# Optimization experiments

Measured on AMD Instinct MI355X. Metric: run time of the kernel, lower is better.

Reference implementation:

```python
import jax, jax.numpy as jnp
import numpy as np

PHI = 0.1  # fraction of pruned weights randomized per inference


def setup_inputs() -> dict:
    key = jax.random.key(0)
    k1, k2, k3 = jax.random.split(key, 3)
    d_out, d_in, batch = 8192, 8192, 256
    W = jax.random.normal(k1, (d_out, d_in), jnp.float32) * 0.02
    prune = jax.random.uniform(k2, (d_out, d_in)) < 0.9
    W = jnp.where(prune, 0.0, W)
    mask = (W == 0.0)  # _register_masks: pruned positions
    x = jax.random.normal(k3, (batch, d_in), jnp.float32)
    return {"x": x, "W": W, "mask": mask}


def reference(x, W, mask):
    # --- _apply_random_flip (vectorized) ---
    n_pruned = int(np.asarray(jnp.sum(mask)))          # concrete mask -> static count
    n_flip = max(1, int(PHI * n_pruned))
    keep = ~mask
    n_keep = jnp.sum(keep).astype(W.dtype)
    wk = jnp.where(keep, W, 0.0)
    mean = jnp.sum(wk) / n_keep
    # torch .std() is unbiased (n-1 denominator)
    var = jnp.sum(jnp.where(keep, (W - mean) ** 2, 0.0)) / (n_keep - 1.0)
    std = jnp.sqrt(var)
    key = jax.random.key(42)
    ks, kv = jax.random.split(key)
    # uniform random permutation of pruned indices -> top_k of random scores
    scores = jnp.where(mask.ravel(), jax.random.uniform(ks, (W.size,)), -1.0)
    _, flip_idx = jax.lax.top_k(scores, n_flip)        # [n_flip] flat indices into W
    vals = jax.random.normal(kv, (n_flip,), W.dtype) * std * 0.1
    W_flipped = W.ravel().at[flip_idx].set(vals).reshape(W.shape)
    # --- base_model forward (Linear, no bias) ---
    out = x @ W_flipped.T                               # [batch, d_out]
    # --- _restore_masks: zero flipped weights again (no effect on out) ---
    _ = jnp.where(mask, 0.0, W_flipped)
    return out
```

## Files before the change

### kernel.cpp

```cpp
#include <hip/hip_runtime.h>

typedef unsigned int u32;
typedef unsigned long long u64;
typedef unsigned short u16;

#define NTOT   67108864u
#define T0P    7399424u
#define PBASE  7226u
#define NSUP   966u
#define SEGN   2048u
#define SEGCAP 4096u
#define SUPCAP 8192u
#define KSPLIT 4

struct Scalars {
  double sumW;
  double sumW2;
  u64 npruned;
  u64 nflip;
  float stdf;
  float pad;
};

#define OFF_GHIST  0ull
#define OFF_ALLOC  4096ull
#define OFF_SBASE  8192ull
#define OFF_SCUR   12288ull
#define OFF_SC     16384ull
#define OFF_SEGCNT 16512ull
#define OFF_XBF    24704ull
#define OFF_SEGS   4219008ull
#define OFF_ROUTED 37773440ull

__host__ __device__ inline void tf2x32(u32 k0, u32 k1, u32 x0, u32 x1, u32& y0, u32& y1) {
  u32 ks2 = k0 ^ k1 ^ 0x1BD11BDAu;
  x0 += k0; x1 += k1;
#define TFR(r) { x0 += x1; x1 = (x1 << (r)) | (x1 >> (32 - (r))); x1 ^= x0; }
  TFR(13) TFR(15) TFR(26) TFR(6)  x0 += k1;  x1 += ks2 + 1u;
  TFR(17) TFR(29) TFR(16) TFR(24) x0 += ks2; x1 += k0 + 2u;
  TFR(13) TFR(15) TFR(26) TFR(6)  x0 += k0;  x1 += k1 + 3u;
  TFR(17) TFR(29) TFR(16) TFR(24) x0 += k1;  x1 += ks2 + 4u;
  TFR(13) TFR(15) TFR(26) TFR(6)  x0 += ks2; x1 += k0 + 5u;
#undef TFR
  y0 = x0; y1 = x1;
}

__device__ inline u32 jax_bits32(u32 k0, u32 k1, u32 i) {
  u32 y0, y1; tf2x32(k0, k1, 0u, i, y0, y1);
  return y0 ^ y1;
}

__device__ inline u16 f2bf(float f) {
  union { float f; u32 u; } c; c.f = f;
  u32 r = ((c.u >> 16) & 1u) + 0x7FFFu;
  return (u16)((c.u + r) >> 16);
}

__device__ inline float erfinv32(float x) {
  float w = -log1pf(-x * x);
  float p;
  if (w < 5.0f) {
    w -= 2.5f;
    p = 2.81022636e-08f;
    p = fmaf(p, w, 3.43273939e-07f);
    p = fmaf(p, w, -3.5233877e-06f);
    p = fmaf(p, w, -4.39150654e-06f);
    p = fmaf(p, w, 0.00021858087f);
    p = fmaf(p, w, -0.00125372503f);
    p = fmaf(p, w, -0.00417768164f);
    p = fmaf(p, w, 0.246640727f);
    p = fmaf(p, w, 1.50140941f);
  } else {
    w = sqrtf(w) - 3.0f;
    p = -0.000200214257f;
    p = fmaf(p, w, 0.000100950558f);
    p = fmaf(p, w, 0.00134934322f);
    p = fmaf(p, w, -0.00367342844f);
    p = fmaf(p, w, 0.00573950773f);
    p = fmaf(p, w, -0.0076224613f);
    p = fmaf(p, w, 0.00943887047f);
    p = fmaf(p, w, 1.00167406f);
    p = fmaf(p, w, 2.83297682f);
  }
  return p * x;
}

__device__ inline void blk_excl_scan_1024(const u32* cnt, u32* excl, u32* wtmp) {
  __syncthreads();
  u32 t = threadIdx.x;
  u32 a0 = cnt[t*4], a1 = cnt[t*4+1], a2 = cnt[t*4+2], a3 = cnt[t*4+3];
  u32 s = a0 + a1 + a2 + a3;
  u32 lane = t & 63, wv = t >> 6;
  u32 inc = s;
  for (int o = 1; o < 64; o <<= 1) { u32 v = (u32)__shfl_up((int)inc, o); if (lane >= (u32)o) inc += v; }
  if (lane == 63) wtmp[wv] = inc;
  __syncthreads();
  u32 woff = 0;
  for (u32 w = 0; w < wv; w++) woff += wtmp[w];
  u32 base = woff + inc - s;
  excl[t*4]   = base;
  excl[t*4+1] = base + a0;
  excl[t*4+2] = base + a0 + a1;
  excl[t*4+3] = base + a0 + a1 + a2;
  __syncthreads();
}

__device__ inline void blk_suffix_scan_1024(const u32* cnt, u32* suf, u32* wtmp) {
  __syncthreads();
  u32 t = threadIdx.x;
  u32 a0 = cnt[1023 - t*4], a1 = cnt[1022 - t*4], a2 = cnt[1021 - t*4], a3 = cnt[1020 - t*4];
  u32 s = a0 + a1 + a2 + a3;
  u32 lane = t & 63, wv = t >> 6;
  u32 inc = s;
  for (int o = 1; o < 64; o <<= 1) { u32 v = (u32)__shfl_up((int)inc, o); if (lane >= (u32)o) inc += v; }
  if (lane == 63) wtmp[wv] = inc;
  __syncthreads();
  u32 woff = 0;
  for (u32 w = 0; w < wv; w++) woff += wtmp[w];
  u32 base = woff + inc - s;
  suf[1023 - t*4] = base;
  suf[1022 - t*4] = base + a0;
  suf[1021 - t*4] = base + a1 + a0;
  suf[1020 - t*4] = base + a2 + a1 + a0;
  __syncthreads();
}

__global__ __launch_bounds__(256) void k_pass1(const float* __restrict__ W, Scalars* sc,
                                               u32* ghist, u32* segcnt, u32* segs,
                                               u32 uk0, u32 uk1) {
  __shared__ u32 lhist[1024];
  __shared__ u32 lcnt, lwr;
  for (u32 j = threadIdx.x; j < 1024; j += 256) lhist[j] = 0;
  if (threadIdx.x == 0) { lcnt = 0; lwr = 0; }
  __syncthreads();
  u32 gid = blockIdx.x * 256 + threadIdx.x;
  u32 stride4 = SEGN * 256 * 4;
  u32 lane = threadIdx.x & 63;
  u64 lt = (lane == 0) ? 0ull : (~0ull >> (64 - lane));
  u32* seg = segs + (u64)blockIdx.x * SEGCAP;
  double s = 0.0, s2 = 0.0; u32 cnt = 0;
  for (u32 b4 = gid * 4; b4 < NTOT; b4 += stride4) {
    float4 wv4 = *(const float4*)(W + b4);
    float we[4] = {wv4.x, wv4.y, wv4.z, wv4.w};
#pragma unroll
    for (int e = 0; e < 4; e++) {
      u32 l = b4 + e;
      float w = we[e];
      s  += (double)w;
      s2 += (double)w * w;
      bool pr = (w == 0.0f);
      cnt += pr ? 1u : 0u;
      u32 sb = jax_bits32(uk0, uk1, l) >> 9;
      bool q = pr && (sb >= T0P);
      u64 m = __ballot(q);
      u32 tot = (u32)__popcll(m);
      if (tot) {
        u32 base = 0;
        if (lane == 0) base = atomicAdd(&lcnt, tot);
        base = (u32)__shfl((int)base, 0);
        if (base + tot <= SEGCAP) {
          if (lane == 0) atomicMax(&lwr, base + tot);
          if (q) {
            seg[base + (u32)__popcll(m & lt)] = l;
            atomicAdd(&lhist[(sb >> 10) - PBASE], 1u);
          }
        }
      }
    }
  }
  for (int o = 32; o > 0; o >>= 1) {
    s += __shfl_down(s, o); s2 += __shfl_down(s2, o); cnt += __shfl_down(cnt, o);
  }
  if (lane == 0) {
    atomicAdd(&sc->sumW, s);
    atomicAdd(&sc->sumW2, s2);
    atomicAdd(&sc->npruned, (u64)cnt);
  }
  __syncthreads();
  for (u32 j = threadIdx.x; j < 1024; j += 256)
    if (j < NSUP && lhist[j]) atomicAdd(&ghist[j], lhist[j]);
  if (threadIdx.x == 0) segcnt[blockIdx.x] = lwr;
}

__global__ __launch_bounds__(256) void k_scan(const u32* __restrict__ ghist, Scalars* sc,
                                              u32* alloc, u32* superbase, u32* supercur) {
  __shared__ u32 h[1024], ex[1024], sb[1024], wtmp[4];
  u32 t = threadIdx.x;
  for (u32 j = t; j < 1024; j += 256) h[j] = ghist[j];
  blk_excl_scan_1024(h, ex, wtmp);
  blk_suffix_scan_1024(h, sb, wtmp);
  for (u32 j = t; j < 1024; j += 256) {
    alloc[j] = ex[j]; superbase[j] = sb[j]; supercur[j] = ex[j];
  }
  if (t == 0) {
    double nk = (double)NTOT - (double)sc->npruned;
    double mean = sc->sumW / nk;
    double var = (sc->sumW2 - 2.0 * mean * sc->sumW + nk * mean * mean) / (nk - 1.0);
    sc->stdf = (float)sqrt(var);
    u64 nfi = (u64)(0.1 * (double)sc->npruned);
    if (nfi < 1) nfi = 1;
    sc->nflip = nfi;
  }
}

__global__ __launch_bounds__(256) void k_route(const u32* __restrict__ segs,
                                               const u32* __restrict__ segcnt,
                                               u32* supercur, u32* routed,
                                               u32 uk0, u32 uk1) {
  __shared__ u32 lbuf[16384];
  __shared__ u16 lp[16384];
  __shared__ u16 inv[16384];
  __shared__ u32 lhist[1024], lbase[1024], gdest[1024], lcur[1024];
  __shared__ u32 wtmp[4];
  u32 t = threadIdx.x;
  for (u32 j = t; j < 1024; j += 256) lhist[j] = 0;
  u32 c0 = segcnt[blockIdx.x*4+0], c1 = segcnt[blockIdx.x*4+1];
  u32 c2 = segcnt[blockIdx.x*4+2], c3 = segcnt[blockIdx.x*4+3];
  u32 off[4] = {0, c0, c0+c1, c0+c1+c2};
  u32 cs[4] = {c0, c1, c2, c3};
  u32 total = c0+c1+c2+c3;
  __syncthreads();
#pragma unroll
  for (int sg = 0; sg < 4; sg++) {
    const u32* sp = segs + ((u64)blockIdx.x*4 + sg) * SEGCAP;
    for (u32 i = t; i < cs[sg]; i += 256) {
      u32 idx = sp[i];
      u32 sb2 = jax_bits32(uk0, uk1, idx) >> 9;
      u32 p = (sb2 >> 10) - PBASE;
      u32 j = off[sg] + i;
      lbuf[j] = idx;
      lp[j] = (u16)p;
      atomicAdd(&lhist[p], 1u);
    }
  }
  blk_excl_scan_1024(lhist, lbase, wtmp);
  for (u32 p = t; p < 1024; p += 256) {
    u32 c = lhist[p];
    if (c) gdest[p] = atomicAdd(&supercur[p], c);
    lcur[p] = lbase[p];
  }
  __syncthreads();
  for (u32 j = t; j < total; j += 256) {
    u32 slot = atomicAdd(&lcur[lp[j]], 1u);
    inv[slot] = (u16)j;
  }
  __syncthreads();
  for (u32 j = t; j < total; j += 256) {
    u32 i = inv[j];
    u32 p = lp[i];
    routed[gdest[p] + (j - lbase[p])] = lbuf[i];
  }
}

__global__ __launch_bounds__(256) void k_rank(float* __restrict__ W,
                                              const u32* __restrict__ ghist,
                                              const u32* __restrict__ alloc,
                                              const u32* __restrict__ superbase,
                                              const u32* __restrict__ routed,
                                              const Scalars* __restrict__ sc,
                                              u32 uk0, u32 uk1, u32 vk0, u32 vk1) {
  u32 p = blockIdx.x;
  u32 n = ghist[p]; if (n == 0) return;
  if (n > SUPCAP) n = SUPCAP;
  u64 nflip = sc->nflip;
  u32 rbase = superbase[p];
  if ((u64)rbase >= nflip) return;
  __shared__ u32 sIdx[SUPCAP];
  __shared__ u16 sFine[SUPCAP];
  __shared__ u32 pIdx[SUPCAP];
  __shared__ u32 hist[1024], gbase[1024], cur[1024];
  __shared__ u32 wtmp[4];
  u32 t = threadIdx.x;
  for (u32 j = t; j < 1024; j += 256) hist[j] = 0;
  __syncthreads();
  const u32* src = routed + alloc[p];
  u32 fbias = (p + PBASE) << 10;
  for (u32 i = t; i < n; i += 256) {
    u32 idx = src[i];
    u32 sb2 = jax_bits32(uk0, uk1, idx) >> 9;
    u32 f = sb2 - fbias;
    sIdx[i] = idx;
    sFine[i] = (u16)f;
    atomicAdd(&hist[f], 1u);
  }
  blk_suffix_scan_1024(hist, gbase, wtmp);
  for (u32 j = t; j < 1024; j += 256) cur[j] = gbase[j];
  __syncthreads();
  for (u32 i = t; i < n; i += 256) {
    u32 pos = atomicAdd(&cur[sFine[i]], 1u);
    pIdx[pos] = sIdx[i];
  }
  __syncthreads();
  float stdf = sc->stdf;
  for (u32 i = t; i < n; i += 256) {
    u32 f = sFine[i];
    u32 g0 = gbase[f], g1 = g0 + hist[f];
    u32 v = sIdx[i];
    u32 ord = 0;
    for (u32 q = g0; q < g1; q++) ord += (pIdx[q] < v) ? 1u : 0u;
    u64 rank = (u64)rbase + gbase[f] + ord;
    if (rank >= nflip) continue;
    u32 bits = jax_bits32(vk0, vk1, (u32)rank);
    union { u32 u; float fl; } cv; cv.u = 0x3F800000u | (bits >> 9);
    float fu = cv.fl - 1.0f;
    const float lo = -0.99999994f;
    float u2 = fmaxf(lo, fu * 2.0f + lo);
    float nrm = 1.41421354f * erfinv32(u2);
    W[v] = (nrm * stdf) * 0.1f;
  }
}

__global__ __launch_bounds__(256) void k_xconv(const float* __restrict__ x, u16* __restrict__ xbf) {
  u32 i = blockIdx.x * blockDim.x + threadIdx.x;
  float4 v = ((const float4*)x)[i];
  ushort4 o; o.x = f2bf(v.x); o.y = f2bf(v.y); o.z = f2bf(v.z); o.w = f2bf(v.w);
  ((ushort4*)xbf)[i] = o;
}

typedef __bf16 bf16x8 __attribute__((ext_vector_type(8)));
typedef float f32x4 __attribute__((ext_vector_type(4)));

__global__ __launch_bounds__(256, 2) void k_gemm(const u16* __restrict__ xbf,
                                                 const float* __restrict__ W,
                                                 float* __restrict__ out) {
  __shared__ u16 xs[256 * 72];
  __shared__ u16 wsm[64 * 72];
  u32 tid = threadIdx.x;
  u32 lane = tid & 63, wv = tid >> 6;
  u32 nt0 = blockIdx.x * 64;
  u32 kbase = blockIdx.y * (8192 / KSPLIT);
  f32x4 acc[4][4];
#pragma unroll
  for (int i = 0; i < 4; i++)
#pragma unroll
    for (int j = 0; j < 4; j++) acc[i][j] = (f32x4){0.f, 0.f, 0.f, 0.f};

  for (u32 kb = kbase; kb < kbase + 2048u; kb += 64u) {
#pragma unroll
    for (int r8 = 0; r8 < 8; r8++) {
      u32 row = r8 * 32 + (tid >> 3);
      u32 kseg = (tid & 7) * 8;
      uint4 v = *(const uint4*)(xbf + (u64)row * 8192 + kb + kseg);
      *(uint4*)&xs[row * 72 + kseg] = v;
    }
#pragma unroll
    for (int r = 0; r < 4; r++) {
      u32 f4 = r * 256 + tid;
      u32 row = f4 >> 4;
      u32 kc = (f4 & 15) * 4;
      float4 v = *(const float4*)(W + (u64)(nt0 + row) * 8192 + kb + kc);
      ushort4 o; o.x = f2bf(v.x); o.y = f2bf(v.y); o.z = f2bf(v.z); o.w = f2bf(v.w);
      *(ushort4*)&wsm[row * 72 + kc] = o;
    }
    __syncthreads();
#pragma unroll
    for (int ks = 0; ks < 2; ks++) {
      bf16x8 a[4], b[4];
      u32 koff = ks * 32 + (lane >> 4) * 8;
      u32 rsel = lane & 15;
#pragma unroll
      for (int mt = 0; mt < 4; mt++) a[mt] = *(bf16x8*)&xs[(wv * 64 + mt * 16 + rsel) * 72 + koff];
#pragma unroll
      for (int nt = 0; nt < 4; nt++) b[nt] = *(bf16x8*)&wsm[(nt * 16 + rsel) * 72 + koff];
#pragma unroll
      for (int mt = 0; mt < 4; mt++)
#pragma unroll
        for (int nt = 0; nt < 4; nt++)
          acc[mt][nt] = __builtin_amdgcn_mfma_f32_16x16x32_bf16(a[mt], b[nt], acc[mt][nt], 0, 0, 0);
    }
    __syncthreads();
  }
  u32 quad = lane >> 4, col = lane & 15;
#pragma unroll
  for (int mt = 0; mt < 4; mt++)
#pragma unroll
    for (int nt = 0; nt < 4; nt++) {
      u32 n = nt0 + nt * 16 + col;
#pragma unroll
      for (int rg = 0; rg < 4; rg++) {
        u32 m = wv * 64 + mt * 16 + quad * 4 + rg;
        atomicAdd(&out[(u64)m * 8192 + n], acc[mt][nt][rg]);
      }
    }
}

extern "C" void kernel_launch(void* const* d_in, const int* in_sizes, int n_in,
                              void* d_out, int out_size, void* d_ws, size_t ws_size,
                              hipStream_t stream) {
  const float* x; float* W;
  if (in_sizes[0] == 2097152) { x = (const float*)d_in[0]; W = (float*)d_in[1]; }
  else                        { x = (const float*)d_in[1]; W = (float*)d_in[0]; }
  float* out = (float*)d_out;
  char* ws = (char*)d_ws;

  u32* ghist     = (u32*)(ws + OFF_GHIST);
  u32* alloc     = (u32*)(ws + OFF_ALLOC);
  u32* superbase = (u32*)(ws + OFF_SBASE);
  u32* supercur  = (u32*)(ws + OFF_SCUR);
  Scalars* sc    = (Scalars*)(ws + OFF_SC);
  u32* segcnt    = (u32*)(ws + OFF_SEGCNT);
  u16* xbf       = (u16*)(ws + OFF_XBF);
  u32* segs      = (u32*)(ws + OFF_SEGS);
  u32* routed    = (u32*)(ws + OFF_ROUTED);

  u32 a0, a1, b0, b1;
  tf2x32(0u, 42u, 0u, 0u, a0, a1);
  tf2x32(0u, 42u, 0u, 1u, b0, b1);

  hipMemsetAsync(ghist, 0, 4096, stream);
  hipMemsetAsync(sc, 0, sizeof(Scalars), stream);
  hipMemsetAsync(out, 0, (size_t)out_size * 4, stream);

  k_xconv<<<2048, 256, 0, stream>>>(x, xbf);
  k_pass1<<<SEGN, 256, 0, stream>>>(W, sc, ghist, segcnt, segs, a0, a1);
  k_scan<<<1, 256, 0, stream>>>(ghist, sc, alloc, superbase, supercur);
  k_route<<<SEGN / 4, 256, 0, stream>>>(segs, segcnt, supercur, routed, a0, a1);
  k_rank<<<NSUP, 256, 0, stream>>>(W, ghist, alloc, superbase, routed, sc, a0, a1, b0, b1);
  dim3 g(128, KSPLIT);
  k_gemm<<<g, 256, 0, stream>>>(xbf, W, out);
}
```

Measured before the change: 1.153 ms.

## Restructure top-k candidate routing into per-wave segments with two-pass deterministic bucketing

Pass1 drops the per-block LDS atomics and ballot-based compaction. Each wave now writes its candidates into its own segment using a wave prefix scan. Routing is split into a histogram pass, a column scan and a scatter pass, with 2048 finer superbuckets, so the large-LDS k_route kernel and its global atomics go away. Rank buckets shrink to 512 fine bins, which lowers shared memory per block and should raise occupancy, at the cost of more kernel launches and an extra read of the segments.

```diff
diff --git a/kernel.cpp b/kernel.cpp
--- a/kernel.cpp
+++ b/kernel.cpp
@@ -6,11 +6,11 @@
 
 #define NTOT   67108864u
 #define T0P    7399424u
-#define PBASE  7226u
-#define NSUP   966u
-#define SEGN   2048u
-#define SEGCAP 4096u
-#define SUPCAP 8192u
+#define PBASE  14452u
+#define NSUP   1932u
+#define NWSEG  4096u
+#define WCAP   2176u
+#define RCAP   4352u
 #define KSPLIT 4
 
 struct Scalars {
@@ -22,15 +22,16 @@
   float pad;
 };
 
-#define OFF_GHIST  0ull
-#define OFF_ALLOC  4096ull
-#define OFF_SBASE  8192ull
-#define OFF_SCUR   12288ull
-#define OFF_SC     16384ull
-#define OFF_SEGCNT 16512ull
-#define OFF_XBF    24704ull
-#define OFF_SEGS   4219008ull
-#define OFF_ROUTED 37773440ull
+#define OFF_COLSUM 0ull
+#define OFF_ALLOC  8192ull
+#define OFF_SBASE  16384ull
+#define OFF_SC     24576ull
+#define OFF_SEGCNT 24704ull
+#define OFF_BHIST  41216ull
+#define OFF_BDEST  2138368ull
+#define OFF_XBF    4235520ull
+#define OFF_SEGS   8429824ull
+#define OFF_ROUTED 44081408ull
 
 __host__ __device__ inline void tf2x32(u32 k0, u32 k1, u32 x0, u32 x1, u32& y0, u32& y1) {
   u32 ks2 = k0 ^ k1 ^ 0x1BD11BDAu;
@@ -85,88 +86,42 @@
   return p * x;
 }
 
-__device__ inline void blk_excl_scan_1024(const u32* cnt, u32* excl, u32* wtmp) {
-  __syncthreads();
+__global__ __launch_bounds__(256) void k_pass1(const float* __restrict__ W, Scalars* sc,
+                                               u32* segcnt, u32* segs, u32 uk0, u32 uk1) {
   u32 t = threadIdx.x;
-  u32 a0 = cnt[t*4], a1 = cnt[t*4+1], a2 = cnt[t*4+2], a3 = cnt[t*4+3];
-  u32 s = a0 + a1 + a2 + a3;
-  u32 lane = t & 63, wv = t >> 6;
-  u32 inc = s;
-  for (int o = 1; o < 64; o <<= 1) { u32 v = (u32)__shfl_up((int)inc, o); if (lane >= (u32)o) inc += v; }
-  if (lane == 63) wtmp[wv] = inc;
-  __syncthreads();
-  u32 woff = 0;
-  for (u32 w = 0; w < wv; w++) woff += wtmp[w];
-  u32 base = woff + inc - s;
-  excl[t*4]   = base;
-  excl[t*4+1] = base + a0;
-  excl[t*4+2] = base + a0 + a1;
-  excl[t*4+3] = base + a0 + a1 + a2;
-  __syncthreads();
-}
-
-__device__ inline void blk_suffix_scan_1024(const u32* cnt, u32* suf, u32* wtmp) {
-  __syncthreads();
-  u32 t = threadIdx.x;
-  u32 a0 = cnt[1023 - t*4], a1 = cnt[1022 - t*4], a2 = cnt[1021 - t*4], a3 = cnt[1020 - t*4];
-  u32 s = a0 + a1 + a2 + a3;
-  u32 lane = t & 63, wv = t >> 6;
-  u32 inc = s;
-  for (int o = 1; o < 64; o <<= 1) { u32 v = (u32)__shfl_up((int)inc, o); if (lane >= (u32)o) inc += v; }
-  if (lane == 63) wtmp[wv] = inc;
-  __syncthreads();
-  u32 woff = 0;
-  for (u32 w = 0; w < wv; w++) woff += wtmp[w];
-  u32 base = woff + inc - s;
-  suf[1023 - t*4] = base;
-  suf[1022 - t*4] = base + a0;
-  suf[1021 - t*4] = base + a1 + a0;
-  suf[1020 - t*4] = base + a2 + a1 + a0;
-  __syncthreads();
-}
-
-__global__ __launch_bounds__(256) void k_pass1(const float* __restrict__ W, Scalars* sc,
-                                               u32* ghist, u32* segcnt, u32* segs,
-                                               u32 uk0, u32 uk1) {
-  __shared__ u32 lhist[1024];
-  __shared__ u32 lcnt, lwr;
-  for (u32 j = threadIdx.x; j < 1024; j += 256) lhist[j] = 0;
-  if (threadIdx.x == 0) { lcnt = 0; lwr = 0; }
-  __syncthreads();
-  u32 gid = blockIdx.x * 256 + threadIdx.x;
-  u32 stride4 = SEGN * 256 * 4;
-  u32 lane = threadIdx.x & 63;
-  u64 lt = (lane == 0) ? 0ull : (~0ull >> (64 - lane));
-  u32* seg = segs + (u64)blockIdx.x * SEGCAP;
+  u32 gid = blockIdx.x * 256 + t;
+  u32 lane = t & 63;
+  u32 wid = gid >> 6;
+  u32* wseg = segs + (u64)wid * WCAP;
+  u32 wbase = 0;
   double s = 0.0, s2 = 0.0; u32 cnt = 0;
+  const u32 stride4 = 1024u * 256u * 4u;
   for (u32 b4 = gid * 4; b4 < NTOT; b4 += stride4) {
-    float4 wv4 = *(const float4*)(W + b4);
-    float we[4] = {wv4.x, wv4.y, wv4.z, wv4.w};
+    float4 w4 = *(const float4*)(W + b4);
+    u32 sb0 = jax_bits32(uk0, uk1, b4 + 0) >> 9;
+    u32 sb1 = jax_bits32(uk0, uk1, b4 + 1) >> 9;
+    u32 sb2 = jax_bits32(uk0, uk1, b4 + 2) >> 9;
+    u32 sb3 = jax_bits32(uk0, uk1, b4 + 3) >> 9;
+    float we[4] = {w4.x, w4.y, w4.z, w4.w};
+    u32 sbv[4] = {sb0, sb1, sb2, sb3};
+    u32 cand[4]; u32 nc = 0;
 #pragma unroll
     for (int e = 0; e < 4; e++) {
-      u32 l = b4 + e;
       float w = we[e];
       s  += (double)w;
-      s2 += (double)w * w;
+      s2 += (double)w * (double)w;
       bool pr = (w == 0.0f);
       cnt += pr ? 1u : 0u;
-      u32 sb = jax_bits32(uk0, uk1, l) >> 9;
-      bool q = pr && (sb >= T0P);
-      u64 m = __ballot(q);
-      u32 tot = (u32)__popcll(m);
-      if (tot) {
-        u32 base = 0;
-        if (lane == 0) base = atomicAdd(&lcnt, tot);
-        base = (u32)__shfl((int)base, 0);
-        if (base + tot <= SEGCAP) {
-          if (lane == 0) atomicMax(&lwr, base + tot);
-          if (q) {
-            seg[base + (u32)__popcll(m & lt)] = l;
-            atomicAdd(&lhist[(sb >> 10) - PBASE], 1u);
-          }
-        }
-      }
-    }
+      if (pr && sbv[e] >= T0P) { cand[nc] = b4 + e; nc++; }
+    }
+    u32 inc = nc;
+#pragma unroll
+    for (int o = 1; o < 64; o <<= 1) { u32 v = (u32)__shfl_up((int)inc, o); if (lane >= (u32)o) inc += v; }
+    u32 tot = (u32)__shfl((int)inc, 63);
+    u32 pos = wbase + inc - nc;
+    for (u32 k2 = 0; k2 < nc; k2++)
+      if (pos + k2 < WCAP) wseg[pos + k2] = cand[k2];
+    wbase += tot;
   }
   for (int o = 32; o > 0; o >>= 1) {
     s += __shfl_down(s, o); s2 += __shfl_down(s2, o); cnt += __shfl_down(cnt, o);
@@ -175,22 +130,82 @@
     atomicAdd(&sc->sumW, s);
     atomicAdd(&sc->sumW2, s2);
     atomicAdd(&sc->npruned, (u64)cnt);
-  }
-  __syncthreads();
-  for (u32 j = threadIdx.x; j < 1024; j += 256)
-    if (j < NSUP && lhist[j]) atomicAdd(&ghist[j], lhist[j]);
-  if (threadIdx.x == 0) segcnt[blockIdx.x] = lwr;
-}
-
-__global__ __launch_bounds__(256) void k_scan(const u32* __restrict__ ghist, Scalars* sc,
-                                              u32* alloc, u32* superbase, u32* supercur) {
-  __shared__ u32 h[1024], ex[1024], sb[1024], wtmp[4];
+    segcnt[wid] = (wbase > WCAP) ? WCAP : wbase;
+  }
+}
+
+__global__ __launch_bounds__(256) void k_route_a(const u32* __restrict__ segs,
+                                                 const u32* __restrict__ segcnt,
+                                                 u32* bhist, u32 uk0, u32 uk1) {
+  __shared__ u32 lhist[2048];
   u32 t = threadIdx.x;
-  for (u32 j = t; j < 1024; j += 256) h[j] = ghist[j];
-  blk_excl_scan_1024(h, ex, wtmp);
-  blk_suffix_scan_1024(h, sb, wtmp);
-  for (u32 j = t; j < 1024; j += 256) {
-    alloc[j] = ex[j]; superbase[j] = sb[j]; supercur[j] = ex[j];
+  for (u32 j = t; j < 2048; j += 256) lhist[j] = 0;
+  __syncthreads();
+#pragma unroll 1
+  for (int sg = 0; sg < 16; sg++) {
+    u32 wid = blockIdx.x * 16 + sg;
+    u32 n = segcnt[wid]; if (n > WCAP) n = WCAP;
+    const u32* sp = segs + (u64)wid * WCAP;
+    for (u32 i = t; i < n; i += 256) {
+      u32 sup = (jax_bits32(uk0, uk1, sp[i]) >> 18) - PBASE;
+      atomicAdd(&lhist[sup], 1u);
+    }
+  }
+  __syncthreads();
+  for (u32 j = t; j < 2048; j += 256) bhist[blockIdx.x * 2048 + j] = lhist[j];
+}
+
+__global__ __launch_bounds__(256) void k_colscan(const u32* __restrict__ bhist,
+                                                 u32* bdest, u32* colsum) {
+  __shared__ u32 wtmp[4];
+  u32 s = blockIdx.x, t = threadIdx.x, lane = t & 63, wv = t >> 6;
+  u32 v = bhist[t * 2048 + s];
+  u32 inc = v;
+#pragma unroll
+  for (int o = 1; o < 64; o <<= 1) { u32 x = (u32)__shfl_up((int)inc, o); if (lane >= (u32)o) inc += x; }
+  if (lane == 63) wtmp[wv] = inc;
+  __syncthreads();
+  u32 woff = 0;
+  for (u32 w = 0; w < wv; w++) woff += wtmp[w];
+  bdest[t * 2048 + s] = woff + inc - v;
+  if (t == 255) colsum[s] = woff + inc;
+}
+
+__global__ __launch_bounds__(256) void k_scan(const u32* __restrict__ colsum, Scalars* sc,
+                                              u32* alloc, u32* sbase) {
+  __shared__ u32 h[2048];
+  __shared__ u32 wtmp[4];
+  u32 t = threadIdx.x, lane = t & 63, wv = t >> 6;
+  for (u32 j = t; j < 2048; j += 256) h[j] = colsum[j];
+  __syncthreads();
+  {
+    u32 a[8]; u32 s8 = 0;
+#pragma unroll
+    for (int k = 0; k < 8; k++) { a[k] = h[t * 8 + k]; s8 += a[k]; }
+    u32 inc = s8;
+#pragma unroll
+    for (int o = 1; o < 64; o <<= 1) { u32 v = (u32)__shfl_up((int)inc, o); if (lane >= (u32)o) inc += v; }
+    if (lane == 63) wtmp[wv] = inc;
+    __syncthreads();
+    u32 woff = 0; for (u32 w = 0; w < wv; w++) woff += wtmp[w];
+    u32 base = woff + inc - s8;
+#pragma unroll
+    for (int k = 0; k < 8; k++) { alloc[t * 8 + k] = base; base += a[k]; }
+    __syncthreads();
+  }
+  {
+    u32 a[8]; u32 s8 = 0;
+#pragma unroll
+    for (int k = 0; k < 8; k++) { a[k] = h[2047 - (t * 8 + k)]; s8 += a[k]; }
+    u32 inc = s8;
+#pragma unroll
+    for (int o = 1; o < 64; o <<= 1) { u32 v = (u32)__shfl_up((int)inc, o); if (lane >= (u32)o) inc += v; }
+    if (lane == 63) wtmp[wv] = inc;
+    __syncthreads();
+    u32 woff = 0; for (u32 w = 0; w < wv; w++) woff += wtmp[w];
+    u32 base = woff + inc - s8;
+#pragma unroll
+    for (int k = 0; k < 8; k++) { sbase[2047 - (t * 8 + k)] = base; base += a[k]; }
   }
   if (t == 0) {
     double nk = (double)NTOT - (double)sc->npruned;
@@ -203,88 +218,77 @@
   }
 }
 
-__global__ __launch_bounds__(256) void k_route(const u32* __restrict__ segs,
-                                               const u32* __restrict__ segcnt,
-                                               u32* supercur, u32* routed,
-                                               u32 uk0, u32 uk1) {
-  __shared__ u32 lbuf[16384];
-  __shared__ u16 lp[16384];
-  __shared__ u16 inv[16384];
-  __shared__ u32 lhist[1024], lbase[1024], gdest[1024], lcur[1024];
-  __shared__ u32 wtmp[4];
+__global__ __launch_bounds__(256) void k_route_b(const u32* __restrict__ segs,
+                                                 const u32* __restrict__ segcnt,
+                                                 const u32* __restrict__ alloc,
+                                                 const u32* __restrict__ bdest,
+                                                 u32* routed, u32 uk0, u32 uk1) {
+  __shared__ u32 lcur[2048];
   u32 t = threadIdx.x;
-  for (u32 j = t; j < 1024; j += 256) lhist[j] = 0;
-  u32 c0 = segcnt[blockIdx.x*4+0], c1 = segcnt[blockIdx.x*4+1];
-  u32 c2 = segcnt[blockIdx.x*4+2], c3 = segcnt[blockIdx.x*4+3];
-  u32 off[4] = {0, c0, c0+c1, c0+c1+c2};
-  u32 cs[4] = {c0, c1, c2, c3};
-  u32 total = c0+c1+c2+c3;
-  __syncthreads();
-#pragma unroll
-  for (int sg = 0; sg < 4; sg++) {
-    const u32* sp = segs + ((u64)blockIdx.x*4 + sg) * SEGCAP;
-    for (u32 i = t; i < cs[sg]; i += 256) {
+  for (u32 j = t; j < 2048; j += 256) lcur[j] = alloc[j] + bdest[blockIdx.x * 2048 + j];
+  __syncthreads();
+#pragma unroll 1
+  for (int sg = 0; sg < 16; sg++) {
+    u32 wid = blockIdx.x * 16 + sg;
+    u32 n = segcnt[wid]; if (n > WCAP) n = WCAP;
+    const u32* sp = segs + (u64)wid * WCAP;
+    for (u32 i = t; i < n; i += 256) {
       u32 idx = sp[i];
-      u32 sb2 = jax_bits32(uk0, uk1, idx) >> 9;
-      u32 p = (sb2 >> 10) - PBASE;
-      u32 j = off[sg] + i;
-      lbuf[j] = idx;
-      lp[j] = (u16)p;
-      atomicAdd(&lhist[p], 1u);
-    }
-  }
-  blk_excl_scan_1024(lhist, lbase, wtmp);
-  for (u32 p = t; p < 1024; p += 256) {
-    u32 c = lhist[p];
-    if (c) gdest[p] = atomicAdd(&supercur[p], c);
-    lcur[p] = lbase[p];
-  }
-  __syncthreads();
-  for (u32 j = t; j < total; j += 256) {
-    u32 slot = atomicAdd(&lcur[lp[j]], 1u);
-    inv[slot] = (u16)j;
-  }
-  __syncthreads();
-  for (u32 j = t; j < total; j += 256) {
-    u32 i = inv[j];
-    u32 p = lp[i];
-    routed[gdest[p] + (j - lbase[p])] = lbuf[i];
-  }
+      u32 sup = (jax_bits32(uk0, uk1, idx) >> 18) - PBASE;
+      u32 pos = atomicAdd(&lcur[sup], 1u);
+      routed[pos] = idx;
+    }
+  }
+}
+
+__device__ inline void suf512(const u32* cnt, u32* suf, u32* wtmp) {
+  u32 t = threadIdx.x, lane = t & 63, wv = t >> 6;
+  u32 a0 = cnt[511 - t * 2], a1 = cnt[510 - t * 2];
+  u32 s = a0 + a1;
+  u32 inc = s;
+#pragma unroll
+  for (int o = 1; o < 64; o <<= 1) { u32 v = (u32)__shfl_up((int)inc, o); if (lane >= (u32)o) inc += v; }
+  if (lane == 63) wtmp[wv] = inc;
+  __syncthreads();
+  u32 woff = 0;
+  for (u32 w = 0; w < wv; w++) woff += wtmp[w];
+  u32 base = woff + inc - s;
+  suf[511 - t * 2] = base;
+  suf[510 - t * 2] = base + a0;
+  __syncthreads();
 }
 
 __global__ __launch_bounds__(256) void k_rank(float* __restrict__ W,
-                                              const u32* __restrict__ ghist,
+                                              const u32* __restrict__ colsum,
                                               const u32* __restrict__ alloc,
-                                              const u32* __restrict__ superbase,
+                                              const u32* __restrict__ sbase,
                                               const u32* __restrict__ routed,
                                               const Scalars* __restrict__ sc,
                                               u32 uk0, u32 uk1, u32 vk0, u32 vk1) {
   u32 p = blockIdx.x;
-  u32 n = ghist[p]; if (n == 0) return;
-  if (n > SUPCAP) n = SUPCAP;
+  u32 n = colsum[p]; if (n == 0) return;
+  if (n > RCAP) n = RCAP;
   u64 nflip = sc->nflip;
-  u32 rbase = superbase[p];
+  u32 rbase = sbase[p];
   if ((u64)rbase >= nflip) return;
-  __shared__ u32 sIdx[SUPCAP];
-  __shared__ u16 sFine[SUPCAP];
-  __shared__ u32 pIdx[SUPCAP];
-  __shared__ u32 hist[1024], gbase[1024], cur[1024];
-  __shared__ u32 wtmp[4];
+  __shared__ u32 sIdx[RCAP];
+  __shared__ u16 sFine[RCAP];
+  __shared__ u32 pIdx[RCAP];
+  __shared__ u32 hist[512], gbase[512], cur[512], wtmp[4];
   u32 t = threadIdx.x;
-  for (u32 j = t; j < 1024; j += 256) hist[j] = 0;
+  for (u32 j = t; j < 512; j += 256) hist[j] = 0;
   __syncthreads();
   const u32* src = routed + alloc[p];
-  u32 fbias = (p + PBASE) << 10;
   for (u32 i = t; i < n; i += 256) {
     u32 idx = src[i];
-    u32 sb2 = jax_bits32(uk0, uk1, idx) >> 9;
-    u32 f = sb2 - fbias;
+    u32 f = (jax_bits32(uk0, uk1, idx) >> 9) & 511u;
     sIdx[i] = idx;
     sFine[i] = (u16)f;
     atomicAdd(&hist[f], 1u);
   }
-  blk_suffix_scan_1024(hist, gbase, wtmp);
-  for (u32 j = t; j < 1024; j += 256) cur[j] = gbase[j];
+  __syncthreads();
+  suf512(hist, gbase, wtmp);
+  for (u32 j = t; j < 512; j += 256) cur[j] = gbase[j];
   __syncthreads();
   for (u32 i = t; i < n; i += 256) {
     u32 pos = atomicAdd(&cur[sFine[i]], 1u);
@@ -298,7 +302,7 @@
     u32 v = sIdx[i];
     u32 ord = 0;
     for (u32 q = g0; q < g1; q++) ord += (pIdx[q] < v) ? 1u : 0u;
-    u64 rank = (u64)rbase + gbase[f] + ord;
+    u64 rank = (u64)rbase + g0 + ord;
     if (rank >= nflip) continue;
     u32 bits = jax_bits32(vk0, vk1, (u32)rank);
     union { u32 u; float fl; } cv; cv.u = 0x3F800000u | (bits >> 9);
@@ -393,29 +397,31 @@
   float* out = (float*)d_out;
   char* ws = (char*)d_ws;
 
-  u32* ghist     = (u32*)(ws + OFF_GHIST);
-  u32* alloc     = (u32*)(ws + OFF_ALLOC);
-  u32* superbase = (u32*)(ws + OFF_SBASE);
-  u32* supercur  = (u32*)(ws + OFF_SCUR);
-  Scalars* sc    = (Scalars*)(ws + OFF_SC);
-  u32* segcnt    = (u32*)(ws + OFF_SEGCNT);
-  u16* xbf       = (u16*)(ws + OFF_XBF);
-  u32* segs      = (u32*)(ws + OFF_SEGS);
-  u32* routed    = (u32*)(ws + OFF_ROUTED);
+  u32* colsum = (u32*)(ws + OFF_COLSUM);
+  u32* alloc  = (u32*)(ws + OFF_ALLOC);
+  u32* sbase  = (u32*)(ws + OFF_SBASE);
+  Scalars* sc = (Scalars*)(ws + OFF_SC);
+  u32* segcnt = (u32*)(ws + OFF_SEGCNT);
+  u32* bhist  = (u32*)(ws + OFF_BHIST);
+  u32* bdest  = (u32*)(ws + OFF_BDEST);
+  u16* xbf    = (u16*)(ws + OFF_XBF);
+  u32* segs   = (u32*)(ws + OFF_SEGS);
+  u32* routed = (u32*)(ws + OFF_ROUTED);
 
   u32 a0, a1, b0, b1;
   tf2x32(0u, 42u, 0u, 0u, a0, a1);
   tf2x32(0u, 42u, 0u, 1u, b0, b1);
 
-  hipMemsetAsync(ghist, 0, 4096, stream);
   hipMemsetAsync(sc, 0, sizeof(Scalars), stream);
   hipMemsetAsync(out, 0, (size_t)out_size * 4, stream);
 
   k_xconv<<<2048, 256, 0, stream>>>(x, xbf);
-  k_pass1<<<SEGN, 256, 0, stream>>>(W, sc, ghist, segcnt, segs, a0, a1);
-  k_scan<<<1, 256, 0, stream>>>(ghist, sc, alloc, superbase, supercur);
-  k_route<<<SEGN / 4, 256, 0, stream>>>(segs, segcnt, supercur, routed, a0, a1);
-  k_rank<<<NSUP, 256, 0, stream>>>(W, ghist, alloc, superbase, routed, sc, a0, a1, b0, b1);
+  k_pass1<<<1024, 256, 0, stream>>>(W, sc, segcnt, segs, a0, a1);
+  k_route_a<<<256, 256, 0, stream>>>(segs, segcnt, bhist, a0, a1);
+  k_colscan<<<2048, 256, 0, stream>>>(bhist, bdest, colsum);
+  k_scan<<<1, 256, 0, stream>>>(colsum, sc, alloc, sbase);
+  k_route_b<<<256, 256, 0, stream>>>(segs, segcnt, alloc, bdest, routed, a0, a1);
+  k_rank<<<NSUP, 256, 0, stream>>>(W, colsum, alloc, sbase, routed, sc, a0, a1, b0, b1);
   dim3 g(128, KSPLIT);
   k_gemm<<<g, 256, 0, stream>>>(xbf, W, out);
 }
```

Result: faster. 1.022 ms (-11.4%).
